# Optimization experiments

Hardware: AMD Instinct MI355X
Metric: run time of the kernel (lower is better)

The kernel has to match this reference:

```python
import jax, jax.numpy as jnp
import numpy as np

IN, HID, OUT = 512, 2048, 128
B, T = 8, 512


def setup_inputs() -> dict:
    key = jax.random.key(0)
    ks = jax.random.split(key, 8)
    k = 1.0 / np.sqrt(HID)  # torch default init scale for RNN/Linear
    u = lambda kk, shape: jax.random.uniform(kk, shape, jnp.float32, -k, k)
    return {
        "x": jax.random.normal(ks[0], (B, T, IN), jnp.float32),
        "W_ih": u(ks[1], (HID, IN)),
        "b_ih": u(ks[2], (HID,)),
        "W_hh": u(ks[3], (HID, HID)),
        "b_hh": u(ks[4], (HID,)),
        "W_out": u(ks[5], (OUT, HID)),
        "b_out": u(ks[6], (OUT,)),
    }


def reference(x, W_ih, b_ih, W_hh, b_hh, W_out, b_out):
    # Pre-project inputs for all timesteps in one big GEMM: [B,T,HID]
    xp = jnp.einsum("bti,hi->bth", x, W_ih) + b_ih + b_hh

    def step(h, xt):  # h: [B,HID], xt: [B,HID]
        h = jnp.tanh(xt + h @ W_hh.T)
        return h, h

    h0 = jnp.zeros((x.shape[0], W_hh.shape[0]), x.dtype)
    _, hs = jax.lax.scan(step, h0, jnp.swapaxes(xp, 0, 1))  # hs: [T,B,HID]
    hs = jnp.swapaxes(hs, 0, 1)  # [B,T,HID]
    return hs @ W_out.T + b_out  # [B,T,OUT]
```

## Files before the change

### kernel.cpp

```cpp
#include <hip/hip_runtime.h>


#define IN_K   512
#define HID    2048
#define OUTN   128
#define BB     8
#define TSTEPS 512
#define NWG    64
#define SENT   0xFF80FF80u

typedef __bf16 bf16x8 __attribute__((ext_vector_type(8)));
typedef unsigned short u16x8 __attribute__((ext_vector_type(8)));
typedef unsigned int u32x4 __attribute__((ext_vector_type(4)));
typedef float f32v4 __attribute__((ext_vector_type(4)));

union Frag8 { u16x8 u; bf16x8 b; u32x4 d; };

__device__ __forceinline__ unsigned short f2bf(float f) {
  unsigned int u = __float_as_uint(f);
  return (unsigned short)((u + 0x7FFFu + ((u >> 16) & 1u)) >> 16);
}

__device__ __forceinline__ float tanh_fast(float x) {
  return 1.0f - 2.0f / (__expf(2.0f * x) + 1.0f);
}

__global__ __launch_bounds__(256)
void sentinel_kernel(u32x4* __restrict__ p) {
  const size_t i = (size_t)blockIdx.x * 256 + threadIdx.x;
  u32x4 v; v[0] = SENT; v[1] = SENT; v[2] = SENT; v[3] = SENT;
  p[i] = v;
}

template<int EPI>
__global__ __launch_bounds__(256, 2)
void gemm_kernel(const void* __restrict__ Aptr, const float* __restrict__ Bptr,
                 const float* __restrict__ bias0, const float* __restrict__ bias1,
                 float* __restrict__ Cout, const int Kdim, const int Ndim)
{
  __shared__ __align__(16) unsigned short As[64][56];
  __shared__ __align__(16) unsigned short Bs[64][56];

  const int m0 = blockIdx.x * 64;
  const int n0 = blockIdx.y * 64;
  const int tid = threadIdx.x;
  const int w = tid >> 6, l = tid & 63;
  const int l15 = l & 15, lk = (l >> 4) * 8;
  const int wm = (w >> 1) * 32, wn = (w & 1) * 32;

  f32v4 acc[2][2];
  #pragma unroll
  for (int mt = 0; mt < 2; ++mt)
    #pragma unroll
    for (int nt = 0; nt < 2; ++nt)
      #pragma unroll
      for (int r = 0; r < 4; ++r) acc[mt][nt][r] = 0.0f;

  for (int k0 = 0; k0 < Kdim; k0 += 32) {
    __syncthreads();
    if (EPI == 0) {
      const float* A = (const float*)Aptr;
      const int r = tid >> 3, c4 = (tid & 7) * 4;
      #pragma unroll
      for (int it = 0; it < 2; ++it) {
        const float4 v = *(const float4*)(A + (size_t)(m0 + r + it * 32) * Kdim + k0 + c4);
        unsigned short* d = &As[r + it * 32][c4];
        d[0] = f2bf(v.x); d[1] = f2bf(v.y); d[2] = f2bf(v.z); d[3] = f2bf(v.w);
      }
    } else {
      const unsigned short* A = (const unsigned short*)Aptr;
      const int r = tid >> 2, c8 = (tid & 3) * 8;
      const u16x8 v = *(const u16x8*)(A + (size_t)(m0 + r) * Kdim + k0 + c8);
      *(u16x8*)&As[r][c8] = v;
    }
    {
      const int r = tid >> 3, c4 = (tid & 7) * 4;
      #pragma unroll
      for (int it = 0; it < 2; ++it) {
        const float4 v = *(const float4*)(Bptr + (size_t)(n0 + r + it * 32) * Kdim + k0 + c4);
        unsigned short* d = &Bs[r + it * 32][c4];
        d[0] = f2bf(v.x); d[1] = f2bf(v.y); d[2] = f2bf(v.z); d[3] = f2bf(v.w);
      }
    }
    __syncthreads();

    Frag8 af[2], bg[2];
    #pragma unroll
    for (int mt = 0; mt < 2; ++mt) af[mt].u = *(const u16x8*)&As[wm + mt * 16 + l15][lk];
    #pragma unroll
    for (int nt = 0; nt < 2; ++nt) bg[nt].u = *(const u16x8*)&Bs[wn + nt * 16 + l15][lk];
    #pragma unroll
    for (int mt = 0; mt < 2; ++mt)
      #pragma unroll
      for (int nt = 0; nt < 2; ++nt)
        acc[mt][nt] = __builtin_amdgcn_mfma_f32_16x16x32_bf16(af[mt].b, bg[nt].b, acc[mt][nt], 0, 0, 0);
  }

  #pragma unroll
  for (int mt = 0; mt < 2; ++mt)
    #pragma unroll
    for (int nt = 0; nt < 2; ++nt)
      #pragma unroll
      for (int r = 0; r < 4; ++r) {
        const int m = m0 + wm + mt * 16 + (l >> 4) * 4 + r;
        const int n = n0 + wn + nt * 16 + l15;
        float v = acc[mt][nt][r];
        if (EPI == 0) {
          v += bias0[n] + bias1[n];
          const int b = m >> 9, t = m & 511;
          Cout[((size_t)t * BB + b) * Ndim + n] = v;
        } else {
          v += bias0[n];
          Cout[(size_t)m * Ndim + n] = v;
        }
      }
}

__global__ __launch_bounds__(256, 1)
void scan_kernel(const float* __restrict__ Whh, const float* __restrict__ xp,
                 unsigned short* __restrict__ hs)
{
  const int g = blockIdx.x;
  const int tid = threadIdx.x;
  const int w = tid >> 6, l = tid & 63;
  const int l15 = l & 15, lk = (l >> 4) * 8;
  const int jbase = g * 32;

  Frag8 Bw[2][16];
  #pragma unroll
  for (int nt = 0; nt < 2; ++nt) {
    const int j = jbase + nt * 16 + l15;
    #pragma unroll
    for (int kc = 0; kc < 16; ++kc) {
      const int k = w * 512 + kc * 32 + lk;
      const float4* p = (const float4*)(Whh + (size_t)j * HID + k);
      const float4 u0 = p[0], u1 = p[1];
      Frag8 f;
      f.u[0] = f2bf(u0.x); f.u[1] = f2bf(u0.y); f.u[2] = f2bf(u0.z); f.u[3] = f2bf(u0.w);
      f.u[4] = f2bf(u1.x); f.u[5] = f2bf(u1.y); f.u[6] = f2bf(u1.z); f.u[7] = f2bf(u1.w);
      Bw[nt][kc] = f;
    }
  }

  __shared__ float red[4][2][16][16];
  const int om = tid >> 4;
  const int oj2 = (tid & 15) * 2;
  const int half = oj2 >> 4, col = oj2 & 15;
  const int arow = l15 & 7;

  for (int t = 0; t < TSTEPS; ++t) {
    float xv0 = 0.f, xv1 = 0.f;
    if (tid < 128) {
      const float2 xv = *(const float2*)(xp + ((size_t)t * BB + om) * HID + jbase + oj2);
      xv0 = xv.x; xv1 = xv.y;
    }

    f32v4 acc0, acc1;
    #pragma unroll
    for (int r = 0; r < 4; ++r) { acc0[r] = 0.f; acc1[r] = 0.f; }

    if (t > 0) {
      const unsigned short* hb = hs + ((size_t)arow * TSTEPS + (t - 1)) * HID + w * 512 + lk;
      Frag8 a[16];
      unsigned int valid = 0;
      do {
        #pragma unroll
        for (int kc = 0; kc < 16; ++kc) {
          if (!(valid & (1u << kc))) {
            asm volatile("global_load_dwordx4 %0, %1, off offset:%2 sc0 sc1"
                         : "=v"(a[kc].d) : "v"(hb), "n"(kc * 64));
          }
        }
        asm volatile("s_waitcnt vmcnt(0)" ::: "memory");
        __builtin_amdgcn_sched_barrier(0);
        #pragma unroll
        for (int kc = 0; kc < 16; ++kc) {
          if (!(valid & (1u << kc))) {
            unsigned int mv = min(min(a[kc].d[0] ^ SENT, a[kc].d[1] ^ SENT),
                                  min(a[kc].d[2] ^ SENT, a[kc].d[3] ^ SENT));
            if (__all(mv != 0u)) {
              valid |= (1u << kc);
              acc0 = __builtin_amdgcn_mfma_f32_16x16x32_bf16(a[kc].b, Bw[0][kc].b, acc0, 0, 0, 0);
              acc1 = __builtin_amdgcn_mfma_f32_16x16x32_bf16(a[kc].b, Bw[1][kc].b, acc1, 0, 0, 0);
            }
          }
        }
      } while (valid != 0xFFFFu);
    }

    #pragma unroll
    for (int r = 0; r < 4; ++r) {
      red[w][0][(l >> 4) * 4 + r][l15] = acc0[r];
      red[w][1][(l >> 4) * 4 + r][l15] = acc1[r];
    }
    __syncthreads();

    if (tid < 128) {
      float s0 = red[0][half][om][col]     + red[1][half][om][col]
               + red[2][half][om][col]     + red[3][half][om][col]     + xv0;
      float s1 = red[0][half][om][col + 1] + red[1][half][om][col + 1]
               + red[2][half][om][col + 1] + red[3][half][om][col + 1] + xv1;
      const float h0 = tanh_fast(s0), h1 = tanh_fast(s1);
      const unsigned int packed = (unsigned int)f2bf(h0) | ((unsigned int)f2bf(h1) << 16);
      unsigned int* hp = (unsigned int*)(hs + ((size_t)om * TSTEPS + t) * HID + jbase + oj2);
      __hip_atomic_store(hp, packed, __ATOMIC_RELAXED, __HIP_MEMORY_SCOPE_AGENT);
    }
    __syncthreads();
  }
}

extern "C" void kernel_launch(void* const* d_in, const int* in_sizes, int n_in,
                              void* d_out, int out_size, void* d_ws, size_t ws_size,
                              hipStream_t stream)
{
  (void)in_sizes; (void)n_in; (void)out_size; (void)ws_size;
  const float* x    = (const float*)d_in[0];
  const float* Wih  = (const float*)d_in[1];
  const float* bih  = (const float*)d_in[2];
  const float* Whh  = (const float*)d_in[3];
  const float* bhh  = (const float*)d_in[4];
  const float* Wout = (const float*)d_in[5];
  const float* bout = (const float*)d_in[6];
  float* out = (float*)d_out;

  char* ws = (char*)d_ws;
  float* xp          = (float*)(ws);
  unsigned short* hs = (unsigned short*)(ws + (size_t)(32 << 20));

  sentinel_kernel<<<dim3(4096), 256, 0, stream>>>((u32x4*)hs);
  gemm_kernel<0><<<dim3(64, 32), 256, 0, stream>>>(x, Wih, bih, bhh, xp, IN_K, HID);
  scan_kernel<<<dim3(NWG), 256, 0, stream>>>(Whh, xp, hs);
  gemm_kernel<1><<<dim3(64, 2), 256, 0, stream>>>(hs, Wout, bout, nullptr, out, HID, OUTN);
}
```

Before: 1.820 ms.

## Repartition RNN scan across 32 workgroups of 8 waves with 64 columns each

Cuts the persistent scan grid from 64 to 32 workgroups, and each now owns 64 hidden columns with 512 threads (8 waves), each wave covering a 256-wide K slice. Each wave loads half as many h fragments per step and issues four MFMAs per fragment instead of two, so global h traffic and the number of polling workgroups drop. In exchange the cross-wave reduction in LDS grows to 8 partial sums, and fewer CUs share the serial per-step work, which may lengthen the critical path.

```diff
diff --git a/kernel.cpp b/kernel.cpp
--- a/kernel.cpp
+++ b/kernel.cpp
@@ -6,7 +6,8 @@
 #define OUTN   128
 #define BB     8
 #define TSTEPS 512
-#define NWG    64
+#define NWG    32
+#define JPW    64
 #define SENT   0xFF80FF80u
 
 typedef __bf16 bf16x8 __attribute__((ext_vector_type(8)));
@@ -116,7 +117,7 @@
       }
 }
 
-__global__ __launch_bounds__(256, 1)
+__global__ __launch_bounds__(512, 2)
 void scan_kernel(const float* __restrict__ Whh, const float* __restrict__ xp,
                  unsigned short* __restrict__ hs)
 {
@@ -124,48 +125,50 @@
   const int tid = threadIdx.x;
   const int w = tid >> 6, l = tid & 63;
   const int l15 = l & 15, lk = (l >> 4) * 8;
-  const int jbase = g * 32;
-
-  Frag8 Bw[2][16];
+  const int jbase = g * JPW;
+
+  Frag8 Bw[4][8];
   #pragma unroll
-  for (int nt = 0; nt < 2; ++nt) {
-    const int j = jbase + nt * 16 + l15;
-    #pragma unroll
-    for (int kc = 0; kc < 16; ++kc) {
-      const int k = w * 512 + kc * 32 + lk;
+  for (int jt = 0; jt < 4; ++jt) {
+    const int j = jbase + jt * 16 + l15;
+    #pragma unroll
+    for (int kc = 0; kc < 8; ++kc) {
+      const int k = w * 256 + kc * 32 + lk;
       const float4* p = (const float4*)(Whh + (size_t)j * HID + k);
       const float4 u0 = p[0], u1 = p[1];
       Frag8 f;
       f.u[0] = f2bf(u0.x); f.u[1] = f2bf(u0.y); f.u[2] = f2bf(u0.z); f.u[3] = f2bf(u0.w);
       f.u[4] = f2bf(u1.x); f.u[5] = f2bf(u1.y); f.u[6] = f2bf(u1.z); f.u[7] = f2bf(u1.w);
-      Bw[nt][kc] = f;
+      Bw[jt][kc] = f;
     }
   }
 
-  __shared__ float red[4][2][16][16];
-  const int om = tid >> 4;
-  const int oj2 = (tid & 15) * 2;
-  const int half = oj2 >> 4, col = oj2 & 15;
+  __shared__ float red[8][4][16][16];
+  const int om = tid >> 5;
+  const int oj2 = (tid & 31) * 2;
+  const int jt_e = oj2 >> 4, col = oj2 & 15;
   const int arow = l15 & 7;
 
   for (int t = 0; t < TSTEPS; ++t) {
     float xv0 = 0.f, xv1 = 0.f;
-    if (tid < 128) {
+    if (tid < 256) {
       const float2 xv = *(const float2*)(xp + ((size_t)t * BB + om) * HID + jbase + oj2);
       xv0 = xv.x; xv1 = xv.y;
     }
 
-    f32v4 acc0, acc1;
-    #pragma unroll
-    for (int r = 0; r < 4; ++r) { acc0[r] = 0.f; acc1[r] = 0.f; }
+    f32v4 acc[4];
+    #pragma unroll
+    for (int jt = 0; jt < 4; ++jt)
+      #pragma unroll
+      for (int r = 0; r < 4; ++r) acc[jt][r] = 0.f;
 
     if (t > 0) {
-      const unsigned short* hb = hs + ((size_t)arow * TSTEPS + (t - 1)) * HID + w * 512 + lk;
-      Frag8 a[16];
+      const unsigned short* hb = hs + ((size_t)arow * TSTEPS + (t - 1)) * HID + w * 256 + lk;
+      Frag8 a[8];
       unsigned int valid = 0;
       do {
         #pragma unroll
-        for (int kc = 0; kc < 16; ++kc) {
+        for (int kc = 0; kc < 8; ++kc) {
           if (!(valid & (1u << kc))) {
             asm volatile("global_load_dwordx4 %0, %1, off offset:%2 sc0 sc1"
                          : "=v"(a[kc].d) : "v"(hb), "n"(kc * 64));
@@ -174,32 +177,35 @@
         asm volatile("s_waitcnt vmcnt(0)" ::: "memory");
         __builtin_amdgcn_sched_barrier(0);
         #pragma unroll
-        for (int kc = 0; kc < 16; ++kc) {
+        for (int kc = 0; kc < 8; ++kc) {
           if (!(valid & (1u << kc))) {
             unsigned int mv = min(min(a[kc].d[0] ^ SENT, a[kc].d[1] ^ SENT),
                                   min(a[kc].d[2] ^ SENT, a[kc].d[3] ^ SENT));
             if (__all(mv != 0u)) {
               valid |= (1u << kc);
-              acc0 = __builtin_amdgcn_mfma_f32_16x16x32_bf16(a[kc].b, Bw[0][kc].b, acc0, 0, 0, 0);
-              acc1 = __builtin_amdgcn_mfma_f32_16x16x32_bf16(a[kc].b, Bw[1][kc].b, acc1, 0, 0, 0);
+              #pragma unroll
+              for (int jt = 0; jt < 4; ++jt)
+                acc[jt] = __builtin_amdgcn_mfma_f32_16x16x32_bf16(a[kc].b, Bw[jt][kc].b, acc[jt], 0, 0, 0);
             }
           }
         }
-      } while (valid != 0xFFFFu);
-    }
-
-    #pragma unroll
-    for (int r = 0; r < 4; ++r) {
-      red[w][0][(l >> 4) * 4 + r][l15] = acc0[r];
-      red[w][1][(l >> 4) * 4 + r][l15] = acc1[r];
-    }
-    __syncthreads();
-
-    if (tid < 128) {
-      float s0 = red[0][half][om][col]     + red[1][half][om][col]
-               + red[2][half][om][col]     + red[3][half][om][col]     + xv0;
-      float s1 = red[0][half][om][col + 1] + red[1][half][om][col + 1]
-               + red[2][half][om][col + 1] + red[3][half][om][col + 1] + xv1;
+      } while (valid != 0xFFu);
+    }
+
+    #pragma unroll
+    for (int jt = 0; jt < 4; ++jt)
+      #pragma unroll
+      for (int r = 0; r < 4; ++r)
+        red[w][jt][(l >> 4) * 4 + r][l15] = acc[jt][r];
+    __syncthreads();
+
+    if (tid < 256) {
+      float s0 = xv0, s1 = xv1;
+      #pragma unroll
+      for (int wv = 0; wv < 8; ++wv) {
+        s0 += red[wv][jt_e][om][col];
+        s1 += red[wv][jt_e][om][col + 1];
+      }
       const float h0 = tanh_fast(s0), h1 = tanh_fast(s1);
       const unsigned int packed = (unsigned int)f2bf(h0) | ((unsigned int)f2bf(h1) << 16);
       unsigned int* hp = (unsigned int*)(hs + ((size_t)om * TSTEPS + t) * HID + jbase + oj2);
@@ -229,6 +235,6 @@
 
   sentinel_kernel<<<dim3(4096), 256, 0, stream>>>((u32x4*)hs);
   gemm_kernel<0><<<dim3(64, 32), 256, 0, stream>>>(x, Wih, bih, bhh, xp, IN_K, HID);
-  scan_kernel<<<dim3(NWG), 256, 0, stream>>>(Whh, xp, hs);
+  scan_kernel<<<dim3(NWG), 512, 0, stream>>>(Whh, xp, hs);
   gemm_kernel<1><<<dim3(64, 2), 256, 0, stream>>>(hs, Wout, bout, nullptr, out, HID, OUTN);
 }
```

Measured after the change: 1.819 ms. About the same (-0.0%).
